# Kernel optimization log

Hardware: AMD Instinct MI355X
Metric: run time of the kernel (lower is better)

## Reference

```python
import jax, jax.numpy as jnp
import numpy as np


def setup_inputs() -> dict:
    key = jax.random.key(0)
    k1, k2 = jax.random.split(key)
    B, C, H, W = 16, 512, 64, 64
    x = jax.random.normal(k1, (B, C, H, W), dtype=jnp.float32)
    gamma = jax.random.normal(k2, (1,), dtype=jnp.float32)
    return {"x": x, "gamma": gamma}


def reference(x, gamma):
    # x: [B, C, H, W]
    B, C, H, W = x.shape
    q = x.reshape(B, C, H * W)              # query = key = value = flattened x
    # energy[b, i, j] = <channel_i, channel_j>  -> [B, C, C]
    energy = jnp.einsum('bin,bjn->bij', q, q)
    # attention = softmax(max(energy, -1) - energy) over last dim
    logits = jnp.max(energy, axis=-1, keepdims=True) - energy
    attention = jax.nn.softmax(logits, axis=-1)
    out = jnp.einsum('bij,bjn->bin', attention, q).reshape(B, C, H, W)
    return gamma * out + x
```

## Files before the change

kernel.cpp:

```cpp
#include <hip/hip_runtime.h>
#include <hip/hip_bf16.h>
#include <cstdint>


typedef short    bf16x8 __attribute__((ext_vector_type(8)));
typedef float    f32x4  __attribute__((ext_vector_type(4)));
typedef uint16_t u16x4  __attribute__((ext_vector_type(4)));
typedef uint16_t u16x8  __attribute__((ext_vector_type(8)));

#define AS1 __attribute__((address_space(1)))
#define AS3 __attribute__((address_space(3)))

__device__ __forceinline__ void load_lds16(const void* g, void* l) {
  __builtin_amdgcn_global_load_lds((const AS1 unsigned int*)g,
                                   (AS3 unsigned int*)l, 16, 0, 0);
}

static constexpr int  BB  = 16, C = 512, N = 4096;
static constexpr long XSZ = (long)BB * C * N;
static constexpr long ESZ = (long)BB * C * C;
static constexpr int  ZSPLIT = 8;

__global__ __launch_bounds__(256) void cam_splitT(
    const float* __restrict__ x, uint16_t* __restrict__ qT) {
  __shared__ uint16_t tile[64][68];
  const int t  = threadIdx.x;
  const int b  = blockIdx.z;
  const int c0 = blockIdx.y * 64;
  const int n0 = blockIdx.x * 64;
  const float* xb  = x  + (long)b * C * N;
  uint16_t*    qTb = qT + (long)b * N * C;
  const int cl = t >> 4;
  const int nl = (t & 15) * 4;
  for (int r = 0; r < 4; ++r) {
    const int  c   = cl + r * 16;
    const long off = (long)(c0 + c) * N + n0 + nl;
    const float4 v = *(const float4*)(xb + off);
    const float vv[4] = {v.x, v.y, v.z, v.w};
    u16x4 hv;
    for (int k = 0; k < 4; ++k) {
      __hip_bfloat16 hb = __float2bfloat16(vv[k]);
      hv[k] = *(uint16_t*)&hb;
    }
    *(u16x4*)&tile[c][nl] = hv;
  }
  __syncthreads();
  for (int r = 0; r < 4; ++r) {
    const int n  = cl + r * 16;
    const int cc = (t & 15) * 4;
    u16x4 o = {tile[cc + 0][n], tile[cc + 1][n], tile[cc + 2][n], tile[cc + 3][n]};
    *(u16x4*)(qTb + (long)(n0 + n) * C + c0 + cc) = o;
  }
}

__device__ __forceinline__ void split4(float4 v, uint2& h, uint2& l) {
  const uint32_t u0 = __float_as_uint(v.x), u1 = __float_as_uint(v.y);
  const uint32_t u2 = __float_as_uint(v.z), u3 = __float_as_uint(v.w);
  const float r0 = v.x - __uint_as_float(u0 & 0xffff0000u);
  const float r1 = v.y - __uint_as_float(u1 & 0xffff0000u);
  const float r2 = v.z - __uint_as_float(u2 & 0xffff0000u);
  const float r3 = v.w - __uint_as_float(u3 & 0xffff0000u);
  h.x = (u0 >> 16) | (u1 & 0xffff0000u);
  h.y = (u2 >> 16) | (u3 & 0xffff0000u);
  l.x = (__float_as_uint(r0) >> 16) | (__float_as_uint(r1) & 0xffff0000u);
  l.y = (__float_as_uint(r2) >> 16) | (__float_as_uint(r3) & 0xffff0000u);
}

__global__ __launch_bounds__(256) void cam_energy(
    const float* __restrict__ x, float* __restrict__ E) {
  __shared__ uint16_t smem[4 * 128 * 32];
  const int tid = threadIdx.x;
  const int wave = tid >> 6, lane = tid & 63;
  const int idx = blockIdx.x;
  const int low = idx & 7, chunk = idx >> 3;
  const int gh = chunk / 10, t = chunk - gh * 10;
  const int g  = gh * 8 + low;
  const int b  = g >> 3, z = g & 7;
  const int ti = (t < 4) ? 0 : (t < 7) ? 1 : (t < 9) ? 2 : 3;
  const int tj = t - ((ti * (9 - ti)) >> 1) + ti;
  const bool diag = (ti == tj);
  const int i0 = ti * 128, j0 = tj * 128;
  const float* xb = x + (long)b * C * N;
  const int sr = tid >> 3;
  const int sc = (tid & 7) * 4;
  const float* pA = xb + (long)(i0 + sr) * N + sc;
  const float* pB = xb + (long)(j0 + sr) * N + sc;
  uint16_t* smAh = smem;
  uint16_t* smAl = smem + 4096;
  uint16_t* smBh = diag ? smem        : smem + 8192;
  uint16_t* smBl = diag ? smem + 4096 : smem + 12288;
  const int wr = wave >> 1, wc = wave & 1;
  const int m16 = lane & 15, q4 = lane >> 4;
  const int usw = (q4 ^ ((m16 >> 1) & 3)) * 8;
  f32x4 acc[4][4] = {};
  const int k0 = z * (N / ZSPLIT), kend = k0 + N / ZSPLIT;
  float4 ra[4], rb[4];
  #pragma unroll
  for (int p = 0; p < 4; ++p) {
    ra[p] = *(const float4*)(pA + k0 + (long)p * 32 * N);
    if (!diag) rb[p] = *(const float4*)(pB + k0 + (long)p * 32 * N);
  }
  for (int kk = k0; kk < kend; kk += 32) {
    #pragma unroll
    for (int p = 0; p < 4; ++p) {
      const int row = p * 32 + sr;
      const int scs = sc ^ (((row >> 1) & 3) << 3);
      uint2 h, l;
      split4(ra[p], h, l);
      *(uint2*)(smAh + row * 32 + scs) = h;
      *(uint2*)(smAl + row * 32 + scs) = l;
      if (!diag) {
        split4(rb[p], h, l);
        *(uint2*)(smem + 8192  + row * 32 + scs) = h;
        *(uint2*)(smem + 12288 + row * 32 + scs) = l;
      }
    }
    __syncthreads();
    const int kn = (kk + 32 < kend) ? kk + 32 : k0;
    #pragma unroll
    for (int p = 0; p < 4; ++p) {
      ra[p] = *(const float4*)(pA + kn + (long)p * 32 * N);
      if (!diag) rb[p] = *(const float4*)(pB + kn + (long)p * 32 * N);
    }
    bf16x8 ah[4], al[4], bh[4], bl[4];
    for (int i = 0; i < 4; ++i) {
      const int r = wr * 64 + i * 16 + m16;
      ah[i] = *(const bf16x8*)(smAh + r * 32 + usw);
      al[i] = *(const bf16x8*)(smAl + r * 32 + usw);
    }
    for (int j = 0; j < 4; ++j) {
      const int r = wc * 64 + j * 16 + m16;
      bh[j] = *(const bf16x8*)(smBh + r * 32 + usw);
      bl[j] = *(const bf16x8*)(smBl + r * 32 + usw);
    }
    for (int i = 0; i < 4; ++i)
      for (int j = 0; j < 4; ++j) {
        acc[i][j] = __builtin_amdgcn_mfma_f32_16x16x32_bf16(ah[i], bh[j], acc[i][j], 0, 0, 0);
        acc[i][j] = __builtin_amdgcn_mfma_f32_16x16x32_bf16(ah[i], bl[j], acc[i][j], 0, 0, 0);
        acc[i][j] = __builtin_amdgcn_mfma_f32_16x16x32_bf16(al[i], bh[j], acc[i][j], 0, 0, 0);
      }
    __syncthreads();
  }
  float* Eb = E + (long)z * ESZ + (long)b * C * C;
  for (int i = 0; i < 4; ++i) {
    const int rb_ = i0 + wr * 64 + i * 16 + q4 * 4;
    for (int j = 0; j < 4; ++j) {
      const int cc = j0 + wc * 64 + j * 16 + m16;
      for (int r = 0; r < 4; ++r)
        Eb[(long)(rb_ + r) * C + cc] = acc[i][j][r];
      if (!diag)
        *(f32x4*)(Eb + (long)cc * C + rb_) = acc[i][j];
    }
  }
}

__global__ __launch_bounds__(256) void cam_softmax(
    const float* __restrict__ E, uint16_t* __restrict__ attn) {
  const int t = threadIdx.x;
  const int wave = t >> 6, lane = t & 63;
  const long row = (long)blockIdx.x * 4 + wave;
  const float* e = E + row * C + lane * 8;
  float vv[8] = {};
  for (int z = 0; z < ZSPLIT; ++z) {
    const float4 a0 = *(const float4*)(e + (long)z * ESZ);
    const float4 a1 = *(const float4*)(e + (long)z * ESZ + 4);
    vv[0] += a0.x; vv[1] += a0.y; vv[2] += a0.z; vv[3] += a0.w;
    vv[4] += a1.x; vv[5] += a1.y; vv[6] += a1.z; vv[7] += a1.w;
  }
  float m = vv[0];
  for (int k = 1; k < 8; ++k) m = fminf(m, vv[k]);
  for (int s = 32; s; s >>= 1) m = fminf(m, __shfl_xor(m, s));
  float w[8], sum = 0.f;
  for (int k = 0; k < 8; ++k) { w[k] = __expf(m - vv[k]); sum += w[k]; }
  for (int s = 32; s; s >>= 1) sum += __shfl_xor(sum, s);
  const float inv = 1.0f / sum;
  u16x8 o;
  for (int k = 0; k < 8; ++k) {
    __hip_bfloat16 h = __float2bfloat16(w[k] * inv);
    o[k] = *(uint16_t*)&h;
  }
  *(u16x8*)(attn + row * C + lane * 8) = o;
}

__global__ __launch_bounds__(256) void cam_pv(
    const uint16_t* __restrict__ attn, const uint16_t* __restrict__ qT,
    const float* __restrict__ x, const float* __restrict__ gamma,
    float* __restrict__ out) {
  __shared__ uint16_t smem[2 * 8192];
  const int t = threadIdx.x;
  const int wave = t >> 6, lane = t & 63;
  const int b  = blockIdx.z;
  const int i0 = blockIdx.y * 128;
  const int n0 = blockIdx.x * 128;
  const uint16_t* Ab = attn + (long)b * C * C;
  const uint16_t* Tb = qT   + (long)b * N * C;
  const int wr = wave >> 1, wc = wave & 1;
  const int m16 = lane & 15, q4 = lane >> 4;
  const int usw = (q4 ^ ((m16 >> 1) & 3)) * 8;
  f32x4 acc[4][4] = {};

  auto stage = [&](int p, int kk) {
    #pragma unroll
    for (int s = 0; s < 2; ++s) {
      const int li  = s * 256 + t;
      const int row = li >> 2;
      const int col = ((li & 3) ^ ((row >> 1) & 3)) * 8;
      uint16_t* lp = smem + p * 8192 + li * 8;
      load_lds16(Ab + (long)(i0 + row) * C + kk + col, lp);
      load_lds16(Tb + (long)(n0 + row) * C + kk + col, lp + 4096);
    }
  };

  stage(0, 0);
  asm volatile("s_waitcnt vmcnt(0)" ::: "memory");
  __builtin_amdgcn_s_barrier();
  constexpr int NK = C / 32;
  for (int tk = 0; tk < NK; ++tk) {
    const int cur = tk & 1;
    if (tk + 1 < NK) stage(cur ^ 1, (tk + 1) * 32);
    const uint16_t* sa = smem + cur * 8192;
    bf16x8 a[4], bv[4];
    #pragma unroll
    for (int i = 0; i < 4; ++i)
      a[i]  = *(const bf16x8*)(sa +        (wr * 64 + i * 16 + m16) * 32 + usw);
    #pragma unroll
    for (int j = 0; j < 4; ++j)
      bv[j] = *(const bf16x8*)(sa + 4096 + (wc * 64 + j * 16 + m16) * 32 + usw);
    asm volatile("s_waitcnt lgkmcnt(0)" ::: "memory");
    __builtin_amdgcn_sched_barrier(0);
    #pragma unroll
    for (int i = 0; i < 4; ++i)
      #pragma unroll
      for (int j = 0; j < 4; ++j)
        acc[i][j] = __builtin_amdgcn_mfma_f32_16x16x32_bf16(a[i], bv[j], acc[i][j], 0, 0, 0);
    asm volatile("s_waitcnt vmcnt(0)" ::: "memory");
    __builtin_amdgcn_s_barrier();
  }
  const float g = gamma[0];
  const float* xb = x   + (long)b * C * N;
  float*       ob = out + (long)b * C * N;
  for (int i = 0; i < 4; ++i) {
    const int rb = i0 + wr * 64 + i * 16 + q4 * 4;
    for (int j = 0; j < 4; ++j) {
      const int cc = n0 + wc * 64 + j * 16 + m16;
      for (int r = 0; r < 4; ++r) {
        const long idx = (long)(rb + r) * N + cc;
        ob[idx] = g * acc[i][j][r] + xb[idx];
      }
    }
  }
}

extern "C" void kernel_launch(void* const* d_in, const int* in_sizes, int n_in,
                              void* d_out, int out_size, void* d_ws, size_t ws_size,
                              hipStream_t stream) {
  const float* x     = (const float*)d_in[0];
  const float* gamma = (const float*)d_in[1];
  float* out = (float*)d_out;
  char*  ws  = (char*)d_ws;
  uint16_t* qT   = (uint16_t*)ws;
  float*    E    = (float*)  (ws + XSZ * 2);
  uint16_t* attn = (uint16_t*)(ws + XSZ * 2 + (long)ZSPLIT * ESZ * 4);

  cam_splitT <<<dim3(N / 64, C / 64, BB), 256, 0, stream>>>(x, qT);
  cam_energy <<<dim3(1280),               256, 0, stream>>>(x, E);
  cam_softmax<<<dim3((BB * C) / 4),       256, 0, stream>>>(E, attn);
  cam_pv     <<<dim3(N / 128, C / 128, BB), 256, 0, stream>>>(attn, qT, x, gamma, out);
}
```

Baseline: 414.8 us.

## Triple-buffer PV pipeline, interleave split-K energy layout, drop LDS transpose

The PV kernel now uses a three-stage LDS ring with two tiles in flight and a partial vmcnt wait, so one barrier per K step replaces the wait-then-barrier that stalled on every load. The split-K energy partials are stored interleaved per row, letting softmax read the eight partials of a row from one contiguous region instead of slices far apart. The bf16 transpose kernel drops its LDS tile, with each thread loading eight channel rows and writing 16-byte transposed vectors directly. The cost is extra LDS per block, which can lower occupancy, and less coalesced reads in the transpose.

```diff
diff --git a/kernel.cpp b/kernel.cpp
--- a/kernel.cpp
+++ b/kernel.cpp
@@ -23,33 +23,27 @@
 
 __global__ __launch_bounds__(256) void cam_splitT(
     const float* __restrict__ x, uint16_t* __restrict__ qT) {
-  __shared__ uint16_t tile[64][68];
   const int t  = threadIdx.x;
   const int b  = blockIdx.z;
-  const int c0 = blockIdx.y * 64;
+  const int c0 = blockIdx.y * 128;
   const int n0 = blockIdx.x * 64;
   const float* xb  = x  + (long)b * C * N;
   uint16_t*    qTb = qT + (long)b * N * C;
-  const int cl = t >> 4;
-  const int nl = (t & 15) * 4;
-  for (int r = 0; r < 4; ++r) {
-    const int  c   = cl + r * 16;
-    const long off = (long)(c0 + c) * N + n0 + nl;
-    const float4 v = *(const float4*)(xb + off);
-    const float vv[4] = {v.x, v.y, v.z, v.w};
-    u16x4 hv;
-    for (int k = 0; k < 4; ++k) {
-      __hip_bfloat16 hb = __float2bfloat16(vv[k]);
-      hv[k] = *(uint16_t*)&hb;
-    }
-    *(u16x4*)&tile[c][nl] = hv;
-  }
-  __syncthreads();
-  for (int r = 0; r < 4; ++r) {
-    const int n  = cl + r * 16;
-    const int cc = (t & 15) * 4;
-    u16x4 o = {tile[cc + 0][n], tile[cc + 1][n], tile[cc + 2][n], tile[cc + 3][n]};
-    *(u16x4*)(qTb + (long)(n0 + n) * C + c0 + cc) = o;
+  const int ci = (t >> 4) * 8;
+  const int nj = (t & 15) * 4;
+  f32x4 v[8];
+  #pragma unroll
+  for (int i = 0; i < 8; ++i)
+    v[i] = *(const f32x4*)(xb + (long)(c0 + ci + i) * N + n0 + nj);
+  #pragma unroll
+  for (int k = 0; k < 4; ++k) {
+    u16x8 o;
+    #pragma unroll
+    for (int i = 0; i < 8; ++i) {
+      __hip_bfloat16 hb = __float2bfloat16(v[i][k]);
+      o[i] = *(uint16_t*)&hb;
+    }
+    *(u16x8*)(qTb + (long)(n0 + nj + k) * C + c0 + ci) = o;
   }
 }
 
@@ -141,15 +135,16 @@
       }
     __syncthreads();
   }
-  float* Eb = E + (long)z * ESZ + (long)b * C * C;
+  float* Eb = E + (long)b * C * C * 8 + (long)z * C;
+  constexpr long RS = 8 * C;
   for (int i = 0; i < 4; ++i) {
     const int rb_ = i0 + wr * 64 + i * 16 + q4 * 4;
     for (int j = 0; j < 4; ++j) {
       const int cc = j0 + wc * 64 + j * 16 + m16;
       for (int r = 0; r < 4; ++r)
-        Eb[(long)(rb_ + r) * C + cc] = acc[i][j][r];
+        Eb[(long)(rb_ + r) * RS + cc] = acc[i][j][r];
       if (!diag)
-        *(f32x4*)(Eb + (long)cc * C + rb_) = acc[i][j];
+        *(f32x4*)(Eb + (long)cc * RS + rb_) = acc[i][j];
     }
   }
 }
@@ -159,13 +154,14 @@
   const int t = threadIdx.x;
   const int wave = t >> 6, lane = t & 63;
   const long row = (long)blockIdx.x * 4 + wave;
-  const float* e = E + row * C + lane * 8;
+  const float* e = E + row * (8 * C) + lane * 8;
   float vv[8] = {};
+  #pragma unroll
   for (int z = 0; z < ZSPLIT; ++z) {
-    const float4 a0 = *(const float4*)(e + (long)z * ESZ);
-    const float4 a1 = *(const float4*)(e + (long)z * ESZ + 4);
-    vv[0] += a0.x; vv[1] += a0.y; vv[2] += a0.z; vv[3] += a0.w;
-    vv[4] += a1.x; vv[5] += a1.y; vv[6] += a1.z; vv[7] += a1.w;
+    const f32x4 a0 = *(const f32x4*)(e + (long)z * C);
+    const f32x4 a1 = *(const f32x4*)(e + (long)z * C + 4);
+    vv[0] += a0[0]; vv[1] += a0[1]; vv[2] += a0[2]; vv[3] += a0[3];
+    vv[4] += a1[0]; vv[5] += a1[1]; vv[6] += a1[2]; vv[7] += a1[3];
   }
   float m = vv[0];
   for (int k = 1; k < 8; ++k) m = fminf(m, vv[k]);
@@ -186,7 +182,7 @@
     const uint16_t* __restrict__ attn, const uint16_t* __restrict__ qT,
     const float* __restrict__ x, const float* __restrict__ gamma,
     float* __restrict__ out) {
-  __shared__ uint16_t smem[2 * 8192];
+  __shared__ uint16_t smem[3 * 8192];
   const int t = threadIdx.x;
   const int wave = t >> 6, lane = t & 63;
   const int b  = blockIdx.z;
@@ -211,13 +207,15 @@
     }
   };
 
+  constexpr int NK = C / 32;
   stage(0, 0);
-  asm volatile("s_waitcnt vmcnt(0)" ::: "memory");
-  __builtin_amdgcn_s_barrier();
-  constexpr int NK = C / 32;
+  stage(1, 32);
   for (int tk = 0; tk < NK; ++tk) {
-    const int cur = tk & 1;
-    if (tk + 1 < NK) stage(cur ^ 1, (tk + 1) * 32);
+    const int cur = tk % 3;
+    if (tk == NK - 1) asm volatile("s_waitcnt vmcnt(0)" ::: "memory");
+    else              asm volatile("s_waitcnt vmcnt(4)" ::: "memory");
+    __builtin_amdgcn_s_barrier();
+    if (tk + 2 < NK) stage((tk + 2) % 3, (tk + 2) * 32);
     const uint16_t* sa = smem + cur * 8192;
     bf16x8 a[4], bv[4];
     #pragma unroll
@@ -233,8 +231,6 @@
       #pragma unroll
       for (int j = 0; j < 4; ++j)
         acc[i][j] = __builtin_amdgcn_mfma_f32_16x16x32_bf16(a[i], bv[j], acc[i][j], 0, 0, 0);
-    asm volatile("s_waitcnt vmcnt(0)" ::: "memory");
-    __builtin_amdgcn_s_barrier();
   }
   const float g = gamma[0];
   const float* xb = x   + (long)b * C * N;
@@ -262,7 +258,7 @@
   float*    E    = (float*)  (ws + XSZ * 2);
   uint16_t* attn = (uint16_t*)(ws + XSZ * 2 + (long)ZSPLIT * ESZ * 4);
 
-  cam_splitT <<<dim3(N / 64, C / 64, BB), 256, 0, stream>>>(x, qT);
+  cam_splitT <<<dim3(N / 64, C / 128, BB), 256, 0, stream>>>(x, qT);
   cam_energy <<<dim3(1280),               256, 0, stream>>>(x, E);
   cam_softmax<<<dim3((BB * C) / 4),       256, 0, stream>>>(E, attn);
   cam_pv     <<<dim3(N / 128, C / 128, BB), 256, 0, stream>>>(attn, qT, x, gamma, out);
```

Measured after the change: 414.5 us. Within noise of the previous version (-0.1%).
